# Kernel tuning notes

Measured on AMD Instinct MI355X. Metric: run time of the kernel, lower is better.

## Reference

```python
import jax, jax.numpy as jnp
import numpy as np

N_NODES = 100000
N_EDGES = 1600000
IN_CH = 128
HID = 32
HEADS = 4
OUT_CH = 32
NEG_SLOPE = 0.2  # PyG GATConv default


def setup_inputs() -> dict:
    key = jax.random.key(0)
    ks = jax.random.split(key, 12)
    s = 0.1
    x = jax.random.normal(ks[0], (N_NODES, IN_CH), dtype=jnp.float32)
    edge_index = jax.random.randint(ks[1], (2, N_EDGES), 0, N_NODES, dtype=jnp.int64)
    # layer 1: in -> heads*hid, concat
    W1 = jax.random.normal(ks[2], (IN_CH, HEADS * HID), dtype=jnp.float32) * s
    a_src1 = jax.random.normal(ks[3], (HEADS, HID), dtype=jnp.float32) * s
    a_dst1 = jax.random.normal(ks[4], (HEADS, HID), dtype=jnp.float32) * s
    b1 = jnp.zeros((HEADS * HID,), dtype=jnp.float32)
    # layer 2: heads*hid -> out, single head, averaged
    W2 = jax.random.normal(ks[5], (HEADS * HID, OUT_CH), dtype=jnp.float32) * s
    a_src2 = jax.random.normal(ks[6], (1, OUT_CH), dtype=jnp.float32) * s
    a_dst2 = jax.random.normal(ks[7], (1, OUT_CH), dtype=jnp.float32) * s
    b2 = jnp.zeros((OUT_CH,), dtype=jnp.float32)
    return {"x": x, "edge_index": edge_index, "W1": W1, "a_src1": a_src1,
            "a_dst1": a_dst1, "b1": b1, "W2": W2, "a_src2": a_src2,
            "a_dst2": a_dst2, "b2": b2}


def _gat_layer(x, src, dst, W, a_s, a_d, b, heads, ch, concat):
    n = x.shape[0]
    h = (x @ W).reshape(n, heads, ch)            # [N,H,C]
    alpha_s = jnp.einsum('nhc,hc->nh', h, a_s)   # [N,H]
    alpha_d = jnp.einsum('nhc,hc->nh', h, a_d)
    e = jax.nn.leaky_relu(alpha_s[src] + alpha_d[dst], NEG_SLOPE)  # [E,H]
    # segment softmax over edges sharing a destination (self-loops guarantee
    # every segment is non-empty)
    m = jax.ops.segment_max(e, dst, num_segments=n)
    ex = jnp.exp(e - m[dst])
    denom = jax.ops.segment_sum(ex, dst, num_segments=n)
    alpha = ex / (denom[dst] + 1e-16)            # [E,H]
    out = jax.ops.segment_sum(alpha[:, :, None] * h[src], dst, num_segments=n)  # [N,H,C]
    out = out.reshape(n, heads * ch) if concat else out.mean(axis=1)
    return out + b


def reference(x, edge_index, W1, a_src1, a_dst1, b1, W2, a_src2, a_dst2, b2):
    n = x.shape[0]
    loop = jnp.arange(n, dtype=edge_index.dtype)
    src = jnp.concatenate([edge_index[0], loop])  # add self-loops (PyG default)
    dst = jnp.concatenate([edge_index[1], loop])
    h = _gat_layer(x, src, dst, W1, a_src1, a_dst1, b1, HEADS, HID, True)
    h = jax.nn.relu(h)
    # dropout(p=0.5) is identity in eval mode
    out = _gat_layer(h, src, dst, W2, a_src2, a_dst2, b2, 1, OUT_CH, False)
    return out
```

## Files before the change

### kernel.cpp

```cpp
#include <hip/hip_runtime.h>
#include <math.h>

#define NEG_SLOPE 0.2f
#define EPB 8192

typedef __attribute__((ext_vector_type(8))) short bf16x8;
typedef __attribute__((ext_vector_type(4))) float f32x4;

__device__ __forceinline__ unsigned pack_bf16x2(float a, float b) {
    unsigned ua = __float_as_uint(a);
    unsigned ub = __float_as_uint(b);
    ua += 0x7FFFu + ((ua >> 16) & 1u);
    ub += 0x7FFFu + ((ub >> 16) & 1u);
    return (ua >> 16) | (ub & 0xFFFF0000u);
}
__device__ __forceinline__ unsigned short bf16r(float f) {
    unsigned u = __float_as_uint(f);
    u += 0x7FFFu + ((u >> 16) & 1u);
    return (unsigned short)(u >> 16);
}
__device__ __forceinline__ float bf_lo(unsigned u) { return __uint_as_float(u << 16); }
__device__ __forceinline__ float bf_hi(unsigned u) { return __uint_as_float(u & 0xFFFF0000u); }

#define SWZ(row, byteoff) ((((row) * 256) + (byteoff)) ^ (((row) & 15) << 4))


__global__ __launch_bounds__(256) void wcvt_kernel(const float* __restrict__ W,
                                                   unsigned short* __restrict__ WT,
                                                   int Nc, int total) {
    int id = blockIdx.x * 256 + threadIdx.x;
    if (id < total) {
        int n = id >> 7, k = id & 127;
        WT[id] = bf16r(W[k * Nc + n]);
    }
}


__global__ __launch_bounds__(256) void gscan_bsum(const int* __restrict__ arr,
                                                  int* __restrict__ psum, int M) {
    __shared__ int red[4];
    int tid = threadIdx.x;
    int idx = blockIdx.x * 256 + tid;
    int v = (idx < M) ? arr[idx] : 0;
    #pragma unroll
    for (int off = 1; off < 64; off <<= 1) v += __shfl_xor(v, off, 64);
    if ((tid & 63) == 0) red[tid >> 6] = v;
    __syncthreads();
    if (tid == 0) psum[blockIdx.x] = red[0] + red[1] + red[2] + red[3];
}

__global__ __launch_bounds__(1024) void gscan_psum(int* __restrict__ psum, int nb) {
    __shared__ int ws[16];
    int tid = threadIdx.x, lane = tid & 63, w = tid >> 6;
    int v = (tid < nb) ? psum[tid] : 0;
    int incl = v;
    #pragma unroll
    for (int off = 1; off < 64; off <<= 1) {
        int t = __shfl_up(incl, off, 64);
        if (lane >= off) incl += t;
    }
    if (lane == 63) ws[w] = incl;
    __syncthreads();
    int wbase = 0;
    #pragma unroll
    for (int j = 0; j < 16; j++) { if (j < w) wbase += ws[j]; }
    if (tid < nb) psum[tid] = wbase + incl - v;
}

__global__ __launch_bounds__(256) void gscan_final(int* __restrict__ arr,
                                                   const int* __restrict__ psum, int M) {
    __shared__ int ws[4];
    int tid = threadIdx.x, lane = tid & 63, w = tid >> 6;
    int idx = blockIdx.x * 256 + tid;
    int v = (idx < M) ? arr[idx] : 0;
    int incl = v;
    #pragma unroll
    for (int off = 1; off < 64; off <<= 1) {
        int t = __shfl_up(incl, off, 64);
        if (lane >= off) incl += t;
    }
    if (lane == 63) ws[w] = incl;
    __syncthreads();
    int wbase = 0;
    #pragma unroll
    for (int j = 0; j < 4; j++) { if (j < w) wbase += ws[j]; }
    if (idx < M) arr[idx] = psum[blockIdx.x] + wbase + incl - v;
}


__global__ __launch_bounds__(256) void p1_hist(const int* __restrict__ dst, int E, int N,
                                               int nblk1, int nbuckets,
                                               int* __restrict__ partial) {
    __shared__ int hist[1024];
    int tid = threadIdx.x;
    for (int i = tid; i < nbuckets; i += 256) hist[i] = 0;
    __syncthreads();
    int base = blockIdx.x * EPB;
    int tot = E + N;
    #pragma unroll
    for (int it = 0; it < EPB / 256; it++) {
        int i = base + it * 256 + tid;
        if (i < tot) {
            int d = (i < E) ? dst[i] : (i - E);
            atomicAdd(&hist[d >> 8], 1);
        }
    }
    __syncthreads();
    for (int b = tid; b < nbuckets; b += 256)
        partial[b * nblk1 + blockIdx.x] = hist[b];
}

__global__ __launch_bounds__(256) void p1_scatter(const int* __restrict__ src,
                                                  const int* __restrict__ dst, int E, int N,
                                                  int nblk1, int nbuckets,
                                                  const int* __restrict__ scanned,
                                                  unsigned* __restrict__ pairs) {
    __shared__ int cursor[1024];
    int tid = threadIdx.x;
    for (int b = tid; b < nbuckets; b += 256)
        cursor[b] = scanned[b * nblk1 + blockIdx.x];
    __syncthreads();
    int base = blockIdx.x * EPB;
    int tot = E + N;
    #pragma unroll
    for (int it = 0; it < EPB / 256; it++) {
        int i = base + it * 256 + tid;
        if (i < tot) {
            int s = (i < E) ? src[i] : (i - E);
            int d = (i < E) ? dst[i] : (i - E);
            int pos = atomicAdd(&cursor[d >> 8], 1);
            pairs[pos] = ((unsigned)(d & 255) << 24) | (unsigned)s;
        }
    }
}

#define P2CAP 8192

__global__ __launch_bounds__(256) void p2_kernel(const unsigned* __restrict__ pairs,
                                                 const int* __restrict__ scanned,
                                                 int nblk1, int nbuckets, int Etot, int N,
                                                 const float4* __restrict__ as4,
                                                 const float4* __restrict__ ad4,
                                                 int* __restrict__ rowptr,
                                                 int* __restrict__ col,
                                                 float4* __restrict__ exa) {
    __shared__ unsigned buf[P2CAP];
    __shared__ int cnt[256];
    __shared__ int cur[256];
    __shared__ int wsum[4];
    int b = blockIdx.x;
    int tid = threadIdx.x, lane = tid & 63, w = tid >> 6;
    int bucketStart = scanned[b * nblk1];
    int bucketEnd = (b + 1 < nbuckets) ? scanned[(b + 1) * nblk1] : Etot;
    int sz = bucketEnd - bucketStart;
    bool inLds = (sz <= P2CAP);
    cnt[tid] = 0;
    if (inLds) {
        for (int i = tid; i < sz; i += 256) buf[i] = pairs[bucketStart + i];
    }
    __syncthreads();
    if (inLds) {
        for (int i = tid; i < sz; i += 256) atomicAdd(&cnt[buf[i] >> 24], 1);
    } else {
        for (int i = bucketStart + tid; i < bucketEnd; i += 256)
            atomicAdd(&cnt[pairs[i] >> 24], 1);
    }
    __syncthreads();
    int v = cnt[tid];
    int incl = v;
    #pragma unroll
    for (int off = 1; off < 64; off <<= 1) {
        int t = __shfl_up(incl, off, 64);
        if (lane >= off) incl += t;
    }
    if (lane == 63) wsum[w] = incl;
    __syncthreads();
    int wbase = 0;
    #pragma unroll
    for (int j = 0; j < 4; j++) { if (j < w) wbase += wsum[j]; }
    int base = bucketStart + wbase + incl - v;
    cur[tid] = base;
    int d = b * 256 + tid;
    if (d < N) rowptr[d] = base;
    if (b == nbuckets - 1 && tid == 0) rowptr[N] = Etot;
    __syncthreads();
    if (inLds) {
        for (int i = tid; i < sz; i += 256) {
            unsigned p = buf[i];
            int dl = p >> 24, s = (int)(p & 0xFFFFFFu);
            int pos = atomicAdd(&cur[dl], 1);
            col[pos] = s;
            float4 A = as4[s];
            float4 D = ad4[b * 256 + dl];
            float4 ex;
            float e;
            e = A.x + D.x; e = fmaxf(e, e * NEG_SLOPE); ex.x = __expf(e);
            e = A.y + D.y; e = fmaxf(e, e * NEG_SLOPE); ex.y = __expf(e);
            e = A.z + D.z; e = fmaxf(e, e * NEG_SLOPE); ex.z = __expf(e);
            e = A.w + D.w; e = fmaxf(e, e * NEG_SLOPE); ex.w = __expf(e);
            exa[pos] = ex;
        }
    } else {
        for (int i = bucketStart + tid; i < bucketEnd; i += 256) {
            unsigned p = pairs[i];
            int dl = p >> 24, s = (int)(p & 0xFFFFFFu);
            int pos = atomicAdd(&cur[dl], 1);
            col[pos] = s;
            float4 A = as4[s];
            float4 D = ad4[b * 256 + dl];
            float4 ex;
            float e;
            e = A.x + D.x; e = fmaxf(e, e * NEG_SLOPE); ex.x = __expf(e);
            e = A.y + D.y; e = fmaxf(e, e * NEG_SLOPE); ex.y = __expf(e);
            e = A.z + D.z; e = fmaxf(e, e * NEG_SLOPE); ex.z = __expf(e);
            e = A.w + D.w; e = fmaxf(e, e * NEG_SLOPE); ex.w = __expf(e);
            exa[pos] = ex;
        }
    }
}


__global__ __launch_bounds__(256) void gemm1_kernel(const float* __restrict__ x,
                                                    const unsigned short* __restrict__ W1T,
                                                    const float* __restrict__ a_s,
                                                    const float* __restrict__ a_d,
                                                    uint4* __restrict__ h1b,
                                                    float* __restrict__ as1,
                                                    float* __restrict__ ad1, int N) {
    __shared__ char xs[16384];
    __shared__ char wsm[32768];
    int tid = threadIdx.x;
    int row0 = blockIdx.x * 64;

    #pragma unroll
    for (int it = 0; it < 8; it++) {
        int idx = it * 256 + tid;
        int n = idx >> 4, kq = idx & 15;
        uint4 v = ((const uint4*)W1T)[idx];
        *(uint4*)(wsm + SWZ(n, kq * 16)) = v;
    }
    #pragma unroll
    for (int it = 0; it < 8; it++) {
        int idx = it * 256 + tid;
        int r = idx >> 5, k4 = idx & 31;
        int row = row0 + r;
        float4 v = (row < N) ? ((const float4*)x)[(size_t)row * 32 + k4]
                             : make_float4(0.f, 0.f, 0.f, 0.f);
        uint2 p;
        p.x = pack_bf16x2(v.x, v.y);
        p.y = pack_bf16x2(v.z, v.w);
        *(uint2*)(xs + SWZ(r, k4 * 8)) = p;
    }
    __syncthreads();

    int wv = tid >> 6, lane = tid & 63;
    int r0 = wv * 16;
    int lm = lane & 15, lk = lane >> 4;

    bf16x8 afr[4];
    #pragma unroll
    for (int ks = 0; ks < 4; ks++) {
        int row = r0 + lm;
        afr[ks] = *(const bf16x8*)(xs + SWZ(row, ks * 64 + lk * 16));
    }
    f32x4 acc[8];
    #pragma unroll
    for (int nt = 0; nt < 8; nt++) acc[nt] = (f32x4){0.f, 0.f, 0.f, 0.f};

    #pragma unroll
    for (int nt = 0; nt < 8; nt++) {
        int c = nt * 16 + lm;
        #pragma unroll
        for (int ks = 0; ks < 4; ks++) {
            bf16x8 bfr = *(const bf16x8*)(wsm + SWZ(c, ks * 64 + lk * 16));
            acc[nt] = __builtin_amdgcn_mfma_f32_16x16x32_bf16(afr[ks], bfr, acc[nt], 0, 0, 0);
        }
    }
    __syncthreads();

    #pragma unroll
    for (int nt = 0; nt < 8; nt++) {
        int c = nt * 16 + lm;
        #pragma unroll
        for (int e = 0; e < 4; e++) {
            int row = r0 + lk * 4 + e;
            *(unsigned short*)(xs + SWZ(row, c * 2)) = bf16r(acc[nt][e]);
        }
    }
    __syncthreads();

    #pragma unroll
    for (int it = 0; it < 4; it++) {
        int idx = it * 256 + tid;
        int row = idx >> 4, q = idx & 15;
        if (row0 + row < N) {
            uint4 v = *(const uint4*)(xs + SWZ(row, q * 16));
            h1b[(size_t)(row0 + row) * 16 + q] = v;
        }
    }
    {
        int row = tid >> 2, h = tid & 3;
        if (row0 + row < N) {
            float sd = 0.f, dd = 0.f;
            #pragma unroll
            for (int q = 0; q < 4; q++) {
                uint4 v = *(const uint4*)(xs + SWZ(row, h * 64 + q * 16));
                unsigned uu[4] = {v.x, v.y, v.z, v.w};
                #pragma unroll
                for (int j = 0; j < 4; j++) {
                    int k = h * 32 + q * 8 + 2 * j;
                    sd = fmaf(bf_lo(uu[j]), a_s[k], sd);
                    sd = fmaf(bf_hi(uu[j]), a_s[k + 1], sd);
                    dd = fmaf(bf_lo(uu[j]), a_d[k], dd);
                    dd = fmaf(bf_hi(uu[j]), a_d[k + 1], dd);
                }
            }
            as1[(row0 + row) * 4 + h] = sd;
            ad1[(row0 + row) * 4 + h] = dd;
        }
    }
}


__global__ __launch_bounds__(256) void agg1_kernel(const int* __restrict__ rowptr,
                                                   const int* __restrict__ col,
                                                   const unsigned* __restrict__ h1b,
                                                   const float* __restrict__ exa,
                                                   const float* __restrict__ b1,
                                                   unsigned* __restrict__ out1b, int N) {
    int lane = threadIdx.x & 63;
    int wid = __builtin_amdgcn_readfirstlane(threadIdx.x >> 6);
    int n = blockIdx.x * 4 + wid;
    if (n >= N) return;
    int hh = lane >> 4;
    int beg = rowptr[n], end = rowptr[n + 1];
    float ax0 = 0.f, ay0 = 0.f, den0 = 0.f;
    float ax1 = 0.f, ay1 = 0.f, den1 = 0.f;
    int i = beg;
    for (; i + 16 <= end; i += 16) {
        int ss[16];
        float ex[16];
        unsigned uu[16];
        #pragma unroll
        for (int j = 0; j < 16; j++) ss[j] = col[i + j];
        #pragma unroll
        for (int j = 0; j < 16; j++) {
            ex[j] = exa[(i + j) * 4 + hh];
            uu[j] = h1b[ss[j] * 64 + lane];
        }
        #pragma unroll
        for (int j = 0; j < 16; j++) {
            if (j & 1) {
                den1 += ex[j];
                ax1 = fmaf(ex[j], bf_lo(uu[j]), ax1);
                ay1 = fmaf(ex[j], bf_hi(uu[j]), ay1);
            } else {
                den0 += ex[j];
                ax0 = fmaf(ex[j], bf_lo(uu[j]), ax0);
                ay0 = fmaf(ex[j], bf_hi(uu[j]), ay0);
            }
        }
    }
    for (; i + 4 <= end; i += 4) {
        int ss[4];
        float ex[4];
        unsigned uu[4];
        #pragma unroll
        for (int j = 0; j < 4; j++) ss[j] = col[i + j];
        #pragma unroll
        for (int j = 0; j < 4; j++) {
            ex[j] = exa[(i + j) * 4 + hh];
            uu[j] = h1b[ss[j] * 64 + lane];
        }
        #pragma unroll
        for (int j = 0; j < 4; j++) {
            den0 += ex[j];
            ax0 = fmaf(ex[j], bf_lo(uu[j]), ax0);
            ay0 = fmaf(ex[j], bf_hi(uu[j]), ay0);
        }
    }
    for (; i < end; i++) {
        int s = col[i];
        float ex = exa[i * 4 + hh];
        unsigned u = h1b[s * 64 + lane];
        den0 += ex;
        ax0 = fmaf(ex, bf_lo(u), ax0);
        ay0 = fmaf(ex, bf_hi(u), ay0);
    }
    float den = den0 + den1, ax = ax0 + ax1, ay = ay0 + ay1;
    float2 bb = ((const float2*)b1)[lane];
    float ox = fmaxf(ax / den + bb.x, 0.f);
    float oy = fmaxf(ay / den + bb.y, 0.f);
    out1b[n * 64 + lane] = pack_bf16x2(ox, oy);
}


__global__ __launch_bounds__(256) void gemm2_kernel(const uint4* __restrict__ out1b,
                                                    const unsigned short* __restrict__ W2T,
                                                    const float* __restrict__ a_s,
                                                    const float* __restrict__ a_d,
                                                    uint4* __restrict__ h2b,
                                                    float* __restrict__ as2,
                                                    float* __restrict__ ad2, int N) {
    __shared__ char xs[16384];
    __shared__ char wsm[8192];
    int tid = threadIdx.x;
    int row0 = blockIdx.x * 64;

    #pragma unroll
    for (int it = 0; it < 2; it++) {
        int idx = it * 256 + tid;
        int n = idx >> 4, kq = idx & 15;
        uint4 v = ((const uint4*)W2T)[idx];
        *(uint4*)(wsm + SWZ(n, kq * 16)) = v;
    }
    #pragma unroll
    for (int it = 0; it < 4; it++) {
        int idx = it * 256 + tid;
        int r = idx >> 4, q = idx & 15;
        int row = row0 + r;
        uint4 v = (row < N) ? out1b[(size_t)row * 16 + q] : make_uint4(0, 0, 0, 0);
        *(uint4*)(xs + SWZ(r, q * 16)) = v;
    }
    __syncthreads();

    int wv = tid >> 6, lane = tid & 63;
    int r0 = wv * 16;
    int lm = lane & 15, lk = lane >> 4;

    bf16x8 afr[4];
    #pragma unroll
    for (int ks = 0; ks < 4; ks++) {
        int row = r0 + lm;
        afr[ks] = *(const bf16x8*)(xs + SWZ(row, ks * 64 + lk * 16));
    }
    f32x4 acc[2];
    acc[0] = (f32x4){0.f, 0.f, 0.f, 0.f};
    acc[1] = (f32x4){0.f, 0.f, 0.f, 0.f};
    #pragma unroll
    for (int nt = 0; nt < 2; nt++) {
        int c = nt * 16 + lm;
        #pragma unroll
        for (int ks = 0; ks < 4; ks++) {
            bf16x8 bfr = *(const bf16x8*)(wsm + SWZ(c, ks * 64 + lk * 16));
            acc[nt] = __builtin_amdgcn_mfma_f32_16x16x32_bf16(afr[ks], bfr, acc[nt], 0, 0, 0);
        }
    }
    __syncthreads();

    #pragma unroll
    for (int nt = 0; nt < 2; nt++) {
        int c = nt * 16 + lm;
        #pragma unroll
        for (int e = 0; e < 4; e++) {
            int row = r0 + lk * 4 + e;
            *(unsigned short*)(xs + SWZ(row, c * 2)) = bf16r(acc[nt][e]);
        }
    }
    __syncthreads();

    {
        int row = tid >> 2, q = tid & 3;
        if (row0 + row < N) {
            uint4 v = *(const uint4*)(xs + SWZ(row, q * 16));
            h2b[(size_t)(row0 + row) * 4 + q] = v;
        }
    }
    if (tid < 64 && row0 + tid < N) {
        float sd = 0.f, dd = 0.f;
        #pragma unroll
        for (int q = 0; q < 4; q++) {
            uint4 v = *(const uint4*)(xs + SWZ(tid, q * 16));
            unsigned uu[4] = {v.x, v.y, v.z, v.w};
            #pragma unroll
            for (int j = 0; j < 4; j++) {
                int k = q * 8 + 2 * j;
                sd = fmaf(bf_lo(uu[j]), a_s[k], sd);
                sd = fmaf(bf_hi(uu[j]), a_s[k + 1], sd);
                dd = fmaf(bf_lo(uu[j]), a_d[k], dd);
                dd = fmaf(bf_hi(uu[j]), a_d[k + 1], dd);
            }
        }
        as2[row0 + tid] = sd;
        ad2[row0 + tid] = dd;
    }
}


#define AGG2_EDGE(u, l)                                            \
    {                                                              \
        float e = l + adn;                                         \
        e = fmaxf(e, e * NEG_SLOPE);                               \
        float ex = __expf(e);                                      \
        den += ex;                                                 \
        a0 = fmaf(ex, bf_lo(u), a0);                               \
        a1 = fmaf(ex, bf_hi(u), a1);                               \
    }

__global__ __launch_bounds__(256) void agg2_kernel(const int* __restrict__ rowptr,
                                                   const int* __restrict__ col,
                                                   const unsigned* __restrict__ h2b,
                                                   const float* __restrict__ as2,
                                                   const float* __restrict__ ad2,
                                                   const float* __restrict__ b2,
                                                   float* __restrict__ out, int N) {
    int lane = threadIdx.x & 63;
    int wid = __builtin_amdgcn_readfirstlane(threadIdx.x >> 6);
    int n = blockIdx.x * 4 + wid;
    if (n >= N) return;
    int q = lane >> 4, c2 = lane & 15;
    float adn = ad2[n];
    int beg = rowptr[n], end = rowptr[n + 1];
    float a0 = 0.f, a1 = 0.f, den = 0.f;
    int i = beg;
    for (; i + 16 <= end; i += 16) {
        int s0 = col[i + q];
        int s1 = col[i + 4 + q];
        int s2 = col[i + 8 + q];
        int s3 = col[i + 12 + q];
        unsigned u0 = h2b[s0 * 16 + c2];
        unsigned u1 = h2b[s1 * 16 + c2];
        unsigned u2 = h2b[s2 * 16 + c2];
        unsigned u3 = h2b[s3 * 16 + c2];
        float l0 = as2[s0], l1 = as2[s1], l2 = as2[s2], l3 = as2[s3];
        AGG2_EDGE(u0, l0) AGG2_EDGE(u1, l1) AGG2_EDGE(u2, l2) AGG2_EDGE(u3, l3)
    }
    for (; i + 4 <= end; i += 4) {
        int s = col[i + q];
        unsigned u = h2b[s * 16 + c2];
        float l = as2[s];
        AGG2_EDGE(u, l)
    }
    if (i + q < end) {
        int s = col[i + q];
        unsigned u = h2b[s * 16 + c2];
        float l = as2[s];
        AGG2_EDGE(u, l)
    }
    den += __shfl_xor(den, 16, 64);
    den += __shfl_xor(den, 32, 64);
    a0 += __shfl_xor(a0, 16, 64);
    a0 += __shfl_xor(a0, 32, 64);
    a1 += __shfl_xor(a1, 16, 64);
    a1 += __shfl_xor(a1, 32, 64);
    if (q == 0) {
        float2 bb = ((const float2*)b2)[c2];
        ((float2*)out)[n * 16 + c2] = make_float2(a0 / den + bb.x, a1 / den + bb.y);
    }
}


extern "C" void kernel_launch(void* const* d_in, const int* in_sizes, int n_in,
                              void* d_out, int out_size, void* d_ws, size_t ws_size,
                              hipStream_t stream) {
    const float* x    = (const float*)d_in[0];
    const int*   ei   = (const int*)d_in[1];
    const float* W1   = (const float*)d_in[2];
    const float* a_s1 = (const float*)d_in[3];
    const float* a_d1 = (const float*)d_in[4];
    const float* b1   = (const float*)d_in[5];
    const float* W2   = (const float*)d_in[6];
    const float* a_s2 = (const float*)d_in[7];
    const float* a_d2 = (const float*)d_in[8];
    const float* b2   = (const float*)d_in[9];

    int N = in_sizes[0] / 128;
    int E = in_sizes[1] / 2;
    const int* srcA = ei;
    const int* dstA = ei + E;
    int Etot = E + N;

    char* ws = (char*)d_ws;
    size_t off = 0;
    auto alloc = [&](size_t bytes) {
        void* p = ws + off;
        off += (bytes + 255) & ~(size_t)255;
        return p;
    };
    unsigned* h1b   = (unsigned*)alloc((size_t)N * 128 * 2);
    unsigned* out1b = (unsigned*)alloc((size_t)N * 128 * 2);
    unsigned* h2b   = (unsigned*)alloc((size_t)N * 32 * 2);
    float* as1      = (float*)alloc((size_t)N * 4 * 4);
    float* ad1      = (float*)alloc((size_t)N * 4 * 4);
    float* as2      = (float*)alloc((size_t)N * 4);
    float* ad2      = (float*)alloc((size_t)N * 4);
    int*   rowptr   = (int*)alloc((size_t)(N + 1) * 4);
    int*   col      = (int*)alloc((size_t)Etot * 4);
    unsigned* pairs = (unsigned*)alloc((size_t)Etot * 4);
    float* exa      = (float*)alloc((size_t)Etot * 16);
    unsigned short* W1T = (unsigned short*)alloc(128 * 128 * 2);
    unsigned short* W2T = (unsigned short*)alloc(32 * 128 * 2);

    int nbuckets = (N + 255) >> 8;
    int nblk1 = (Etot + EPB - 1) / EPB;
    int M = nbuckets * nblk1;
    int*   partial = (int*)alloc((size_t)M * 4);
    int nbs = (M + 255) / 256;
    int*   psum    = (int*)alloc((size_t)1024 * 4);

    hipLaunchKernelGGL(wcvt_kernel, dim3(64), dim3(256), 0, stream, W1, W1T, 128, 16384);
    hipLaunchKernelGGL(wcvt_kernel, dim3(16), dim3(256), 0, stream, W2, W2T, 32, 4096);
    hipLaunchKernelGGL(gemm1_kernel, dim3((N + 63) / 64), dim3(256), 0, stream,
                       x, W1T, a_s1, a_d1, (uint4*)h1b, as1, ad1, N);

    hipLaunchKernelGGL(p1_hist, dim3(nblk1), dim3(256), 0, stream,
                       dstA, E, N, nblk1, nbuckets, partial);
    hipLaunchKernelGGL(gscan_bsum, dim3(nbs), dim3(256), 0, stream, partial, psum, M);
    hipLaunchKernelGGL(gscan_psum, dim3(1), dim3(1024), 0, stream, psum, nbs);
    hipLaunchKernelGGL(gscan_final, dim3(nbs), dim3(256), 0, stream, partial, psum, M);
    hipLaunchKernelGGL(p1_scatter, dim3(nblk1), dim3(256), 0, stream,
                       srcA, dstA, E, N, nblk1, nbuckets, partial, pairs);
    hipLaunchKernelGGL(p2_kernel, dim3(nbuckets), dim3(256), 0, stream,
                       pairs, partial, nblk1, nbuckets, Etot, N,
                       (const float4*)as1, (const float4*)ad1, rowptr, col, (float4*)exa);

    hipLaunchKernelGGL(agg1_kernel, dim3((N + 3) / 4), dim3(256), 0, stream,
                       rowptr, col, h1b, exa, b1, out1b, N);
    hipLaunchKernelGGL(gemm2_kernel, dim3((N + 63) / 64), dim3(256), 0, stream,
                       (const uint4*)out1b, W2T, a_s2, a_d2, (uint4*)h2b, as2, ad2, N);
    hipLaunchKernelGGL(agg2_kernel, dim3((N + 3) / 4), dim3(256), 0, stream,
                       rowptr, col, h2b, as2, ad2, b2, (float*)d_out, N);
}
```

Measured before the change: 234.0 us.

## Split edge-score computation into separate kernel and widen aggregation loads

Moves the per-edge leaky-relu/exp score computation out of the CSR bucket kernel into a new edge-parallel kernel, which reads col plus a new per-edge destination array and writes exa coalesced instead of scattered. Both aggregation kernels switch to 8-byte per-lane feature loads, so each wavefront processes two (layer 1) or eight (layer 2) edges at once and combines the partial sums with cross-lane shuffles. This trades an extra kernel launch and an extra Etot-sized int array write/read for coalesced score writes and more memory-level parallelism in the gather loops.

Result: no change. 231.5 us (-1.1%).

```diff
diff --git a/kernel.cpp b/kernel.cpp
--- a/kernel.cpp
+++ b/kernel.cpp
@@ -139,11 +139,9 @@
 __global__ __launch_bounds__(256) void p2_kernel(const unsigned* __restrict__ pairs,
                                                  const int* __restrict__ scanned,
                                                  int nblk1, int nbuckets, int Etot, int N,
-                                                 const float4* __restrict__ as4,
-                                                 const float4* __restrict__ ad4,
                                                  int* __restrict__ rowptr,
                                                  int* __restrict__ col,
-                                                 float4* __restrict__ exa) {
+                                                 int* __restrict__ edst) {
     __shared__ unsigned buf[P2CAP];
     __shared__ int cnt[256];
     __shared__ int cur[256];
@@ -187,35 +185,40 @@
     if (inLds) {
         for (int i = tid; i < sz; i += 256) {
             unsigned p = buf[i];
-            int dl = p >> 24, s = (int)(p & 0xFFFFFFu);
+            int dl = p >> 24;
             int pos = atomicAdd(&cur[dl], 1);
-            col[pos] = s;
-            float4 A = as4[s];
-            float4 D = ad4[b * 256 + dl];
-            float4 ex;
-            float e;
-            e = A.x + D.x; e = fmaxf(e, e * NEG_SLOPE); ex.x = __expf(e);
-            e = A.y + D.y; e = fmaxf(e, e * NEG_SLOPE); ex.y = __expf(e);
-            e = A.z + D.z; e = fmaxf(e, e * NEG_SLOPE); ex.z = __expf(e);
-            e = A.w + D.w; e = fmaxf(e, e * NEG_SLOPE); ex.w = __expf(e);
-            exa[pos] = ex;
+            col[pos] = (int)(p & 0xFFFFFFu);
+            edst[pos] = b * 256 + dl;
         }
     } else {
         for (int i = bucketStart + tid; i < bucketEnd; i += 256) {
             unsigned p = pairs[i];
-            int dl = p >> 24, s = (int)(p & 0xFFFFFFu);
+            int dl = p >> 24;
             int pos = atomicAdd(&cur[dl], 1);
-            col[pos] = s;
-            float4 A = as4[s];
-            float4 D = ad4[b * 256 + dl];
-            float4 ex;
-            float e;
-            e = A.x + D.x; e = fmaxf(e, e * NEG_SLOPE); ex.x = __expf(e);
-            e = A.y + D.y; e = fmaxf(e, e * NEG_SLOPE); ex.y = __expf(e);
-            e = A.z + D.z; e = fmaxf(e, e * NEG_SLOPE); ex.z = __expf(e);
-            e = A.w + D.w; e = fmaxf(e, e * NEG_SLOPE); ex.w = __expf(e);
-            exa[pos] = ex;
-        }
+            col[pos] = (int)(p & 0xFFFFFFu);
+            edst[pos] = b * 256 + dl;
+        }
+    }
+}
+
+
+__global__ __launch_bounds__(256) void exk_kernel(const int* __restrict__ col,
+                                                  const int* __restrict__ edst,
+                                                  const float4* __restrict__ as4,
+                                                  const float4* __restrict__ ad4,
+                                                  float4* __restrict__ exa, int Etot) {
+    int i = blockIdx.x * 256 + threadIdx.x;
+    if (i < Etot) {
+        int s = col[i], d = edst[i];
+        float4 A = as4[s];
+        float4 D = ad4[d];
+        float4 ex;
+        float e;
+        e = A.x + D.x; e = fmaxf(e, e * NEG_SLOPE); ex.x = __expf(e);
+        e = A.y + D.y; e = fmaxf(e, e * NEG_SLOPE); ex.y = __expf(e);
+        e = A.z + D.z; e = fmaxf(e, e * NEG_SLOPE); ex.z = __expf(e);
+        e = A.w + D.w; e = fmaxf(e, e * NEG_SLOPE); ex.w = __expf(e);
+        exa[i] = ex;
     }
 }
 
@@ -322,76 +325,76 @@
 }
 
 
+#define A1SLOT(u, ex)                                              \
+    {                                                              \
+        den += ex;                                                 \
+        a0 = fmaf(ex, bf_lo(u.x), a0);                             \
+        a1 = fmaf(ex, bf_hi(u.x), a1);                             \
+        a2 = fmaf(ex, bf_lo(u.y), a2);                             \
+        a3 = fmaf(ex, bf_hi(u.y), a3);                             \
+    }
+
 __global__ __launch_bounds__(256) void agg1_kernel(const int* __restrict__ rowptr,
                                                    const int* __restrict__ col,
-                                                   const unsigned* __restrict__ h1b,
+                                                   const uint2* __restrict__ h1v,
                                                    const float* __restrict__ exa,
                                                    const float* __restrict__ b1,
-                                                   unsigned* __restrict__ out1b, int N) {
+                                                   uint2* __restrict__ out1v, int N) {
     int lane = threadIdx.x & 63;
     int wid = __builtin_amdgcn_readfirstlane(threadIdx.x >> 6);
     int n = blockIdx.x * 4 + wid;
     if (n >= N) return;
-    int hh = lane >> 4;
+    int half = lane >> 5;
+    int cl = lane & 31;
+    int hh = cl >> 3;
     int beg = rowptr[n], end = rowptr[n + 1];
-    float ax0 = 0.f, ay0 = 0.f, den0 = 0.f;
-    float ax1 = 0.f, ay1 = 0.f, den1 = 0.f;
+    float a0 = 0.f, a1 = 0.f, a2 = 0.f, a3 = 0.f, den = 0.f;
     int i = beg;
     for (; i + 16 <= end; i += 16) {
-        int ss[16];
-        float ex[16];
-        unsigned uu[16];
-        #pragma unroll
-        for (int j = 0; j < 16; j++) ss[j] = col[i + j];
-        #pragma unroll
-        for (int j = 0; j < 16; j++) {
-            ex[j] = exa[(i + j) * 4 + hh];
-            uu[j] = h1b[ss[j] * 64 + lane];
-        }
-        #pragma unroll
-        for (int j = 0; j < 16; j++) {
-            if (j & 1) {
-                den1 += ex[j];
-                ax1 = fmaf(ex[j], bf_lo(uu[j]), ax1);
-                ay1 = fmaf(ex[j], bf_hi(uu[j]), ay1);
-            } else {
-                den0 += ex[j];
-                ax0 = fmaf(ex[j], bf_lo(uu[j]), ax0);
-                ay0 = fmaf(ex[j], bf_hi(uu[j]), ay0);
-            }
-        }
-    }
-    for (; i + 4 <= end; i += 4) {
-        int ss[4];
-        float ex[4];
-        unsigned uu[4];
-        #pragma unroll
-        for (int j = 0; j < 4; j++) ss[j] = col[i + j];
-        #pragma unroll
-        for (int j = 0; j < 4; j++) {
-            ex[j] = exa[(i + j) * 4 + hh];
-            uu[j] = h1b[ss[j] * 64 + lane];
-        }
-        #pragma unroll
-        for (int j = 0; j < 4; j++) {
-            den0 += ex[j];
-            ax0 = fmaf(ex[j], bf_lo(uu[j]), ax0);
-            ay0 = fmaf(ex[j], bf_hi(uu[j]), ay0);
-        }
-    }
-    for (; i < end; i++) {
+        int e0 = i + half,      e1 = i + 2 + half,  e2 = i + 4 + half,  e3 = i + 6 + half;
+        int e4 = i + 8 + half,  e5 = i + 10 + half, e6 = i + 12 + half, e7 = i + 14 + half;
+        int s0 = col[e0], s1 = col[e1], s2 = col[e2], s3 = col[e3];
+        int s4 = col[e4], s5 = col[e5], s6 = col[e6], s7 = col[e7];
+        uint2 u0 = h1v[s0 * 32 + cl], u1 = h1v[s1 * 32 + cl];
+        uint2 u2 = h1v[s2 * 32 + cl], u3 = h1v[s3 * 32 + cl];
+        uint2 u4 = h1v[s4 * 32 + cl], u5 = h1v[s5 * 32 + cl];
+        uint2 u6 = h1v[s6 * 32 + cl], u7 = h1v[s7 * 32 + cl];
+        float x0 = exa[e0 * 4 + hh], x1 = exa[e1 * 4 + hh];
+        float x2 = exa[e2 * 4 + hh], x3 = exa[e3 * 4 + hh];
+        float x4 = exa[e4 * 4 + hh], x5 = exa[e5 * 4 + hh];
+        float x6 = exa[e6 * 4 + hh], x7 = exa[e7 * 4 + hh];
+        A1SLOT(u0, x0) A1SLOT(u1, x1) A1SLOT(u2, x2) A1SLOT(u3, x3)
+        A1SLOT(u4, x4) A1SLOT(u5, x5) A1SLOT(u6, x6) A1SLOT(u7, x7)
+    }
+    for (; i + 2 <= end; i += 2) {
+        int e = i + half;
+        int s = col[e];
+        uint2 u = h1v[s * 32 + cl];
+        float x = exa[e * 4 + hh];
+        A1SLOT(u, x)
+    }
+    if (i < end && half == 0) {
         int s = col[i];
-        float ex = exa[i * 4 + hh];
-        unsigned u = h1b[s * 64 + lane];
-        den0 += ex;
-        ax0 = fmaf(ex, bf_lo(u), ax0);
-        ay0 = fmaf(ex, bf_hi(u), ay0);
-    }
-    float den = den0 + den1, ax = ax0 + ax1, ay = ay0 + ay1;
-    float2 bb = ((const float2*)b1)[lane];
-    float ox = fmaxf(ax / den + bb.x, 0.f);
-    float oy = fmaxf(ay / den + bb.y, 0.f);
-    out1b[n * 64 + lane] = pack_bf16x2(ox, oy);
+        uint2 u = h1v[s * 32 + cl];
+        float x = exa[i * 4 + hh];
+        A1SLOT(u, x)
+    }
+    den += __shfl_xor(den, 32, 64);
+    a0 += __shfl_xor(a0, 32, 64);
+    a1 += __shfl_xor(a1, 32, 64);
+    a2 += __shfl_xor(a2, 32, 64);
+    a3 += __shfl_xor(a3, 32, 64);
+    if (half == 0) {
+        float4 bb = ((const float4*)b1)[cl];
+        float o0 = fmaxf(a0 / den + bb.x, 0.f);
+        float o1 = fmaxf(a1 / den + bb.y, 0.f);
+        float o2 = fmaxf(a2 / den + bb.z, 0.f);
+        float o3 = fmaxf(a3 / den + bb.w, 0.f);
+        uint2 pk;
+        pk.x = pack_bf16x2(o0, o1);
+        pk.y = pack_bf16x2(o2, o3);
+        out1v[n * 32 + cl] = pk;
+    }
 }
 
 
@@ -487,19 +490,21 @@
 }
 
 
-#define AGG2_EDGE(u, l)                                            \
+#define A2SLOT(u, l)                                               \
     {                                                              \
         float e = l + adn;                                         \
         e = fmaxf(e, e * NEG_SLOPE);                               \
         float ex = __expf(e);                                      \
         den += ex;                                                 \
-        a0 = fmaf(ex, bf_lo(u), a0);                               \
-        a1 = fmaf(ex, bf_hi(u), a1);                               \
+        a0 = fmaf(ex, bf_lo(u.x), a0);                             \
+        a1 = fmaf(ex, bf_hi(u.x), a1);                             \
+        a2 = fmaf(ex, bf_lo(u.y), a2);                             \
+        a3 = fmaf(ex, bf_hi(u.y), a3);                             \
     }
 
 __global__ __launch_bounds__(256) void agg2_kernel(const int* __restrict__ rowptr,
                                                    const int* __restrict__ col,
-                                                   const unsigned* __restrict__ h2b,
+                                                   const uint2* __restrict__ h2v,
                                                    const float* __restrict__ as2,
                                                    const float* __restrict__ ad2,
                                                    const float* __restrict__ b2,
@@ -508,44 +513,44 @@
     int wid = __builtin_amdgcn_readfirstlane(threadIdx.x >> 6);
     int n = blockIdx.x * 4 + wid;
     if (n >= N) return;
-    int q = lane >> 4, c2 = lane & 15;
+    int q8 = lane >> 3;
+    int cl = lane & 7;
     float adn = ad2[n];
     int beg = rowptr[n], end = rowptr[n + 1];
-    float a0 = 0.f, a1 = 0.f, den = 0.f;
+    float a0 = 0.f, a1 = 0.f, a2 = 0.f, a3 = 0.f, den = 0.f;
     int i = beg;
     for (; i + 16 <= end; i += 16) {
-        int s0 = col[i + q];
-        int s1 = col[i + 4 + q];
-        int s2 = col[i + 8 + q];
-        int s3 = col[i + 12 + q];
-        unsigned u0 = h2b[s0 * 16 + c2];
-        unsigned u1 = h2b[s1 * 16 + c2];
-        unsigned u2 = h2b[s2 * 16 + c2];
-        unsigned u3 = h2b[s3 * 16 + c2];
-        float l0 = as2[s0], l1 = as2[s1], l2 = as2[s2], l3 = as2[s3];
-        AGG2_EDGE(u0, l0) AGG2_EDGE(u1, l1) AGG2_EDGE(u2, l2) AGG2_EDGE(u3, l3)
-    }
-    for (; i + 4 <= end; i += 4) {
-        int s = col[i + q];
-        unsigned u = h2b[s * 16 + c2];
-        float l = as2[s];
-        AGG2_EDGE(u, l)
-    }
-    if (i + q < end) {
-        int s = col[i + q];
-        unsigned u = h2b[s * 16 + c2];
-        float l = as2[s];
-        AGG2_EDGE(u, l)
-    }
+        int e0 = i + q8, e1 = i + 8 + q8;
+        int s0 = col[e0], s1 = col[e1];
+        uint2 u0 = h2v[s0 * 8 + cl];
+        uint2 u1 = h2v[s1 * 8 + cl];
+        float l0 = as2[s0], l1 = as2[s1];
+        A2SLOT(u0, l0) A2SLOT(u1, l1)
+    }
+    for (; i < end; i += 8) {
+        int e = i + q8;
+        if (e < end) {
+            int s = col[e];
+            uint2 u = h2v[s * 8 + cl];
+            float l = as2[s];
+            A2SLOT(u, l)
+        }
+    }
+    den += __shfl_xor(den, 8, 64);
     den += __shfl_xor(den, 16, 64);
     den += __shfl_xor(den, 32, 64);
-    a0 += __shfl_xor(a0, 16, 64);
-    a0 += __shfl_xor(a0, 32, 64);
-    a1 += __shfl_xor(a1, 16, 64);
-    a1 += __shfl_xor(a1, 32, 64);
-    if (q == 0) {
-        float2 bb = ((const float2*)b2)[c2];
-        ((float2*)out)[n * 16 + c2] = make_float2(a0 / den + bb.x, a1 / den + bb.y);
+    a0 += __shfl_xor(a0, 8, 64);  a0 += __shfl_xor(a0, 16, 64);  a0 += __shfl_xor(a0, 32, 64);
+    a1 += __shfl_xor(a1, 8, 64);  a1 += __shfl_xor(a1, 16, 64);  a1 += __shfl_xor(a1, 32, 64);
+    a2 += __shfl_xor(a2, 8, 64);  a2 += __shfl_xor(a2, 16, 64);  a2 += __shfl_xor(a2, 32, 64);
+    a3 += __shfl_xor(a3, 8, 64);  a3 += __shfl_xor(a3, 16, 64);  a3 += __shfl_xor(a3, 32, 64);
+    if (q8 == 0) {
+        float4 bb = ((const float4*)b2)[cl];
+        float4 o;
+        o.x = a0 / den + bb.x;
+        o.y = a1 / den + bb.y;
+        o.z = a2 / den + bb.z;
+        o.w = a3 / den + bb.w;
+        ((float4*)out)[n * 8 + cl] = o;
     }
 }
 
@@ -586,6 +591,7 @@
     float* ad2      = (float*)alloc((size_t)N * 4);
     int*   rowptr   = (int*)alloc((size_t)(N + 1) * 4);
     int*   col      = (int*)alloc((size_t)Etot * 4);
+    int*   edst     = (int*)alloc((size_t)Etot * 4);
     unsigned* pairs = (unsigned*)alloc((size_t)Etot * 4);
     float* exa      = (float*)alloc((size_t)Etot * 16);
     unsigned short* W1T = (unsigned short*)alloc(128 * 128 * 2);
@@ -611,13 +617,15 @@
     hipLaunchKernelGGL(p1_scatter, dim3(nblk1), dim3(256), 0, stream,
                        srcA, dstA, E, N, nblk1, nbuckets, partial, pairs);
     hipLaunchKernelGGL(p2_kernel, dim3(nbuckets), dim3(256), 0, stream,
-                       pairs, partial, nblk1, nbuckets, Etot, N,
-                       (const float4*)as1, (const float4*)ad1, rowptr, col, (float4*)exa);
+                       pairs, partial, nblk1, nbuckets, Etot, N, rowptr, col, edst);
+
+    hipLaunchKernelGGL(exk_kernel, dim3((Etot + 255) / 256), dim3(256), 0, stream,
+                       col, edst, (const float4*)as1, (const float4*)ad1, (float4*)exa, Etot);
 
     hipLaunchKernelGGL(agg1_kernel, dim3((N + 3) / 4), dim3(256), 0, stream,
-                       rowptr, col, h1b, exa, b1, out1b, N);
+                       rowptr, col, (const uint2*)h1b, exa, b1, (uint2*)out1b, N);
     hipLaunchKernelGGL(gemm2_kernel, dim3((N + 63) / 64), dim3(256), 0, stream,
                        (const uint4*)out1b, W2T, a_s2, a_d2, (uint4*)h2b, as2, ad2, N);
     hipLaunchKernelGGL(agg2_kernel, dim3((N + 3) / 4), dim3(256), 0, stream,
-                       rowptr, col, h2b, as2, ad2, b2, (float*)d_out, N);
-}
+                       rowptr, col, (const uint2*)h2b, as2, ad2, b2, (float*)d_out, N);
+}
```
